# Optimization experiments

Measured on AMD Instinct MI355X. Metric: run time of the kernel, lower is better.

The kernel has to match this reference:

```python
import jax, jax.numpy as jnp
import numpy as np

B, H, W, DIM, R = 8, 64, 64, 768, 16
_DN = ('NHWC', 'HWIO', 'NHWC')


def _conv(x, k):
    # stride-1 SAME conv == torch Conv2d(padding=k//2) for 3x3 and 1x1 kernels
    return jax.lax.conv_general_dilated(x, k, (1, 1), 'SAME', dimension_numbers=_DN)


def setup_inputs() -> dict:
    key = jax.random.key(0)
    ks = jax.random.split(key, 16)
    s = 0.02
    return {
        'x': jax.random.normal(ks[0], (B, H, W, DIM), jnp.float32),
        'W_qkv': jax.random.normal(ks[1], (DIM, 3 * DIM), jnp.float32) * s,
        'b_qkv': jax.random.normal(ks[2], (3 * DIM,), jnp.float32) * s,
        'Wa_q': jax.random.normal(ks[3], (DIM, R), jnp.float32) * s,
        'Wb_q': jax.random.normal(ks[4], (R, DIM), jnp.float32) * s,
        'Wa_v': jax.random.normal(ks[5], (DIM, R), jnp.float32) * s,
        'Wb_v': jax.random.normal(ks[6], (R, DIM), jnp.float32) * s,
        'K_q3': jax.random.normal(ks[7], (3, 3, R, R), jnp.float32) * s,
        'b_q3': jax.random.normal(ks[8], (R,), jnp.float32) * s,
        'K_v3': jax.random.normal(ks[9], (3, 3, R, R), jnp.float32) * s,
        'b_v3': jax.random.normal(ks[10], (R,), jnp.float32) * s,
        'K_q1': jax.random.normal(ks[11], (1, 1, R, R), jnp.float32) * s,
        'b_q1': jax.random.normal(ks[12], (R,), jnp.float32) * s,
        'K_v1': jax.random.normal(ks[13], (1, 1, R, R), jnp.float32) * s,
        'b_v1': jax.random.normal(ks[14], (R,), jnp.float32) * s,
    }


def reference(x, W_qkv, b_qkv, Wa_q, Wb_q, Wa_v, Wb_v,
              K_q3, b_q3, K_v3, b_v3, K_q1, b_q1, K_v1, b_v1):
    dim = x.shape[-1]
    # base QKV projection: [B,H,W,3*dim]
    qkv = jnp.einsum('bhwc,cd->bhwd', x, W_qkv) + b_qkv
    # low-rank down-projections: [B,H,W,r]
    a_q = x @ Wa_q
    a_v = x @ Wa_v
    # NHWC convs replace the permute->conv->permute dance in the torch code
    mid_q = _conv(a_q, K_q3) + b_q3 + _conv(a_q, K_q1) + b_q1 + a_q
    mid_v = _conv(a_v, K_v3) + b_v3 + _conv(a_v, K_v1) + b_v1 + a_v
    new_q = mid_q @ Wb_q  # [B,H,W,dim]
    new_v = mid_v @ Wb_v
    qkv = qkv.at[..., :dim].add(new_q)
    qkv = qkv.at[..., -dim:].add(new_v)
    return qkv
```

## Files before the change

### kernel.cpp

```cpp
#include <hip/hip_runtime.h>

typedef __bf16 bf16;
typedef __attribute__((ext_vector_type(8))) __bf16 bf16x8;
typedef __attribute__((ext_vector_type(4))) float f32x4;

#define AS1U(p) ((const __attribute__((address_space(1))) unsigned int*)(p))
#define AS3U(p) ((__attribute__((address_space(3))) unsigned int*)(p))

__device__ __forceinline__ unsigned short f2bf(float f) {
    union { float f; unsigned int u; } a; a.f = f;
    unsigned int u = a.u;
    u += 0x7fffu + ((u >> 16) & 1u);
    return (unsigned short)(u >> 16);
}
__device__ __forceinline__ unsigned int pk2(float a, float b) {
    return (unsigned int)f2bf(a) | ((unsigned int)f2bf(b) << 16);
}

#define MTOT 32768
#define DIM  768
#define KP   832
#define NOUT 2304

__global__ __launch_bounds__(256) void bbuild_kernel(
    const float* __restrict__ Wqkv, const float* __restrict__ Wbq,
    const float* __restrict__ Wbv, const float* __restrict__ Waq,
    const float* __restrict__ Wav, unsigned short* __restrict__ Bt,
    unsigned short* __restrict__ WaT)
{
    const int bx = blockIdx.x;
    const int t = threadIdx.x;
    if (bx < 432) {
        __shared__ float Ts[64][65];
        const int kt = bx % 12, nt = bx / 12;
        #pragma unroll
        for (int it = 0; it < 4; ++it) {
            int idx = it * 256 + t;
            int kr = idx >> 4;
            int nc = (idx & 15) * 4;
            float4 v = *(const float4*)(Wqkv + (size_t)(kt * 64 + kr) * NOUT + nt * 64 + nc);
            Ts[kr][nc + 0] = v.x; Ts[kr][nc + 1] = v.y;
            Ts[kr][nc + 2] = v.z; Ts[kr][nc + 3] = v.w;
        }
        __syncthreads();
        #pragma unroll
        for (int it = 0; it < 4; ++it) {
            int idx = it * 256 + t;
            int nr = idx >> 4;
            int kc = (idx & 15) * 4;
            ushort4 u;
            u.x = f2bf(Ts[kc + 0][nr]); u.y = f2bf(Ts[kc + 1][nr]);
            u.z = f2bf(Ts[kc + 2][nr]); u.w = f2bf(Ts[kc + 3][nr]);
            *(ushort4*)(Bt + (size_t)(nt * 64 + nr) * KP + kt * 64 + kc) = u;
        }
    } else if (bx < 576) {
        int idx = (bx - 432) * 256 + t;
        int n = idx >> 4;
        int k = 768 + (idx & 15) * 4;
        ushort4 u;
        unsigned short* up = (unsigned short*)&u;
        #pragma unroll
        for (int j = 0; j < 4; ++j) {
            int kk = k + j;
            float v = 0.f;
            if (kk < 784) { if (n < 768) v = Wbq[(size_t)(kk - 768) * 768 + n]; }
            else if (kk < 800) { if (n >= 1536) v = Wbv[(size_t)(kk - 784) * 768 + (n - 1536)]; }
            up[j] = f2bf(v);
        }
        *(ushort4*)(Bt + (size_t)n * KP + k) = u;
    } else {
        int idx = (bx - 576) * 256 + t;
        int n = idx / 768, k = idx % 768;
        float v = (n < 16) ? Waq[(size_t)k * 16 + n] : Wav[(size_t)k * 16 + (n - 16)];
        WaT[(size_t)n * 768 + k] = f2bf(v);
    }
}

__global__ __launch_bounds__(256) void prep_kernel(
    const float* __restrict__ x, const bf16* __restrict__ WaT,
    unsigned short* __restrict__ Ap, float* __restrict__ aq, float* __restrict__ av)
{
    __shared__ bf16 Xs[64 * 64];
    const int t = threadIdx.x;
    const int wave = t >> 6, lane = t & 63;
    const int l15 = lane & 15, q = lane >> 4;
    const int p0 = blockIdx.x * 64;
    const int row = t >> 2, c16 = (t & 3) * 16;
    const int r8 = row & 7, ch0 = c16 >> 3;
    f32x4 acc[2] = {};

    for (int kt = 0; kt < 12; ++kt) {
        const float* xp = x + (size_t)(p0 + row) * DIM + kt * 64 + c16;
        float4 v0 = *(const float4*)(xp + 0);
        float4 v1 = *(const float4*)(xp + 4);
        float4 v2 = *(const float4*)(xp + 8);
        float4 v3 = *(const float4*)(xp + 12);
        uint4 u0, u1;
        u0.x = pk2(v0.x, v0.y); u0.y = pk2(v0.z, v0.w);
        u0.z = pk2(v1.x, v1.y); u0.w = pk2(v1.z, v1.w);
        u1.x = pk2(v2.x, v2.y); u1.y = pk2(v2.z, v2.w);
        u1.z = pk2(v3.x, v3.y); u1.w = pk2(v3.z, v3.w);
        unsigned short* apq = Ap + (size_t)(p0 + row) * KP + kt * 64 + c16;
        *(uint4*)(apq) = u0;
        *(uint4*)(apq + 8) = u1;
        __syncthreads();
        *(uint4*)(Xs + row * 64 + ((ch0 + 0) ^ r8) * 8) = u0;
        *(uint4*)(Xs + row * 64 + ((ch0 + 1) ^ r8) * 8) = u1;
        __syncthreads();
        bf16x8 bfr[2][2];
        #pragma unroll
        for (int kk = 0; kk < 2; ++kk)
            #pragma unroll
            for (int nf = 0; nf < 2; ++nf)
                bfr[kk][nf] = *(const bf16x8*)(WaT + (size_t)(nf * 16 + l15) * 768
                                               + kt * 64 + kk * 32 + q * 8);
        #pragma unroll
        for (int kk = 0; kk < 2; ++kk) {
            int phys = ((kk << 2) + q) ^ (l15 & 7);
            bf16x8 af = *(const bf16x8*)(Xs + (wave * 16 + l15) * 64 + phys * 8);
            acc[0] = __builtin_amdgcn_mfma_f32_16x16x32_bf16(af, bfr[kk][0], acc[0], 0, 0, 0);
            acc[1] = __builtin_amdgcn_mfma_f32_16x16x32_bf16(af, bfr[kk][1], acc[1], 0, 0, 0);
        }
    }
    const int m = wave * 16 + q * 4;
    #pragma unroll
    for (int r = 0; r < 4; ++r) {
        aq[(size_t)(p0 + m + r) * 16 + l15] = acc[0][r];
        av[(size_t)(p0 + m + r) * 16 + l15] = acc[1][r];
    }
    uint4 z; z.x = z.y = z.z = z.w = 0u;
    *(uint4*)(Ap + (size_t)(p0 + row) * KP + 800 + (t & 3) * 8) = z;
}

__global__ __launch_bounds__(256) void conv_mid_kernel(
    const float* __restrict__ aq, const float* __restrict__ av,
    const float* __restrict__ Kq3, const float* __restrict__ bq3,
    const float* __restrict__ Kv3, const float* __restrict__ bv3,
    const float* __restrict__ Kq1, const float* __restrict__ bq1,
    const float* __restrict__ Kv1, const float* __restrict__ bv1,
    unsigned short* __restrict__ Ap)
{
    const int bx = blockIdx.x;
    const int qv   = bx & 1;
    const int tile = (bx >> 1) & 15;
    const int b    = bx >> 5;
    const float* a  = qv ? av  : aq;
    const float* K3 = qv ? Kv3 : Kq3;
    const float* K1 = qv ? Kv1 : Kq1;
    const float* b3 = qv ? bv3 : bq3;
    const float* b1 = qv ? bv1 : bq1;

    __shared__ float K3s[9][16][16];
    __shared__ float K1s[16][16];
    const int t = threadIdx.x;
    for (int i = t; i < 9 * 256; i += 256) ((float*)K3s)[i] = K3[i];
    ((float*)K1s)[t] = K1[t];
    __syncthreads();

    const int lh = t >> 4, lw = t & 15;
    const int h = (tile >> 2) * 16 + lh;
    const int w = (tile & 3) * 16 + lw;

    float acc[16];
    const float* ac = a + (((size_t)b * 64 + h) * 64 + w) * 16;
    float cen[16];
    #pragma unroll
    for (int i4 = 0; i4 < 4; ++i4) {
        float4 qd = ((const float4*)ac)[i4];
        cen[i4 * 4 + 0] = qd.x; cen[i4 * 4 + 1] = qd.y;
        cen[i4 * 4 + 2] = qd.z; cen[i4 * 4 + 3] = qd.w;
    }
    #pragma unroll
    for (int o = 0; o < 16; ++o) acc[o] = b3[o] + b1[o] + cen[o];
    #pragma unroll
    for (int i = 0; i < 16; ++i) {
        float vi = cen[i];
        #pragma unroll
        for (int o = 0; o < 16; ++o) acc[o] += vi * K1s[i][o];
    }
    for (int dh = -1; dh <= 1; ++dh) {
        for (int dw = -1; dw <= 1; ++dw) {
            int hh = h + dh, ww = w + dw;
            if ((unsigned)hh < 64u && (unsigned)ww < 64u) {
                const float* ap = a + (((size_t)b * 64 + hh) * 64 + ww) * 16;
                float v[16];
                #pragma unroll
                for (int i4 = 0; i4 < 4; ++i4) {
                    float4 qd = ((const float4*)ap)[i4];
                    v[i4 * 4 + 0] = qd.x; v[i4 * 4 + 1] = qd.y;
                    v[i4 * 4 + 2] = qd.z; v[i4 * 4 + 3] = qd.w;
                }
                const int tap = (dh + 1) * 3 + (dw + 1);
                #pragma unroll
                for (int i = 0; i < 16; ++i) {
                    float vi = v[i];
                    #pragma unroll
                    for (int o = 0; o < 16; ++o) acc[o] += vi * K3s[tap][i][o];
                }
            }
        }
    }
    unsigned short* dst = Ap + (((size_t)b * 64 + h) * 64 + w) * KP + 768 + qv * 16;
    #pragma unroll
    for (int o4 = 0; o4 < 4; ++o4) {
        ushort4 u;
        u.x = f2bf(acc[o4 * 4 + 0]); u.y = f2bf(acc[o4 * 4 + 1]);
        u.z = f2bf(acc[o4 * 4 + 2]); u.w = f2bf(acc[o4 * 4 + 3]);
        *(ushort4*)(dst + o4 * 4) = u;
    }
}

__global__ __launch_bounds__(512, 2) void gemm_kernel(
    const bf16* __restrict__ A, const bf16* __restrict__ Bt,
    const float* __restrict__ bias, float* __restrict__ out)
{
    __shared__ bf16 As[2][256 * 64];
    __shared__ bf16 Bs[2][256 * 64];
    const int t = threadIdx.x;
    const int wave = t >> 6, lane = t & 63;
    const int wm = wave >> 2, wn = wave & 3;
    const int m0 = blockIdx.y * 256, n0 = blockIdx.x * 256;

    const int sr8 = lane >> 3;
    const int slc = (lane & 7) ^ sr8;
    const bf16* gA = A  + (size_t)(m0 + wave * 8 + sr8) * KP + slc * 8;
    const bf16* gB = Bt + (size_t)(n0 + wave * 8 + sr8) * KP + slc * 8;
    const int ldsbase = wave * 512 + lane * 8;

    const int l15 = lane & 15;
    const int q   = lane >> 4;
    const int l7  = lane & 7;

    f32x4 acc[8][4] = {};

    auto STAGE = [&](int kt1, int bufi) {
        const int k0 = kt1 * 64;
        #pragma unroll
        for (int it = 0; it < 4; ++it) {
            __builtin_amdgcn_global_load_lds(AS1U(gA + (size_t)(it * 64) * KP + k0),
                AS3U(&As[bufi][it * 4096 + ldsbase]), 16, 0, 0);
            __builtin_amdgcn_global_load_lds(AS1U(gB + (size_t)(it * 64) * KP + k0),
                AS3U(&Bs[bufi][it * 4096 + ldsbase]), 16, 0, 0);
        }
    };

    STAGE(0, 0);

    for (int kt = 0; kt < 13; ++kt) {
        const int cur = kt & 1;
        __builtin_amdgcn_sched_barrier(0);
        if (kt < 12) {
            STAGE(kt + 1, cur ^ 1);
            asm volatile("s_waitcnt vmcnt(8)" ::: "memory");
        } else {
            asm volatile("s_waitcnt vmcnt(0)" ::: "memory");
        }
        __builtin_amdgcn_s_barrier();

        const bf16* as = &As[cur][0];
        const bf16* bs = &Bs[cur][0];

        bf16x8 bfr[2][4];
        #pragma unroll
        for (int kk = 0; kk < 2; ++kk) {
            const int phys = ((kk << 2) + q) ^ l7;
            #pragma unroll
            for (int ni = 0; ni < 4; ++ni)
                bfr[kk][ni] = *(const bf16x8*)(bs + (wn * 64 + ni * 16 + l15) * 64 + phys * 8);
        }

        #pragma unroll
        for (int p = 0; p < 4; ++p) {
            bf16x8 af[2][2];
            #pragma unroll
            for (int j = 0; j < 2; ++j) {
                const int mi = p * 2 + j;
                #pragma unroll
                for (int kk = 0; kk < 2; ++kk) {
                    const int phys = ((kk << 2) + q) ^ l7;
                    af[j][kk] = *(const bf16x8*)(as + (wm * 128 + mi * 16 + l15) * 64 + phys * 8);
                }
            }
            __builtin_amdgcn_s_barrier();
            asm volatile("s_waitcnt lgkmcnt(0)" ::: "memory");
            __builtin_amdgcn_s_setprio(1);
            #pragma unroll
            for (int j = 0; j < 2; ++j)
                #pragma unroll
                for (int ni = 0; ni < 4; ++ni)
                    #pragma unroll
                    for (int kk = 0; kk < 2; ++kk)
                        acc[p * 2 + j][ni] = __builtin_amdgcn_mfma_f32_16x16x32_bf16(
                            af[j][kk], bfr[kk][ni], acc[p * 2 + j][ni], 0, 0, 0);
            __builtin_amdgcn_s_setprio(0);
            __builtin_amdgcn_s_barrier();
        }
    }

    #pragma unroll
    for (int ni = 0; ni < 4; ++ni) {
        const int col = n0 + wn * 64 + ni * 16 + l15;
        const float bv = bias[col];
        #pragma unroll
        for (int mi = 0; mi < 8; ++mi) {
            const int rbase = m0 + wm * 128 + mi * 16 + (q << 2);
            #pragma unroll
            for (int r = 0; r < 4; ++r)
                out[(size_t)(rbase + r) * NOUT + col] = acc[mi][ni][r] + bv;
        }
    }
}

extern "C" void kernel_launch(void* const* d_in, const int* in_sizes, int n_in,
                              void* d_out, int out_size, void* d_ws, size_t ws_size,
                              hipStream_t stream) {
    const float* x    = (const float*)d_in[0];
    const float* Wqkv = (const float*)d_in[1];
    const float* bqkv = (const float*)d_in[2];
    const float* Waq  = (const float*)d_in[3];
    const float* Wbq  = (const float*)d_in[4];
    const float* Wav  = (const float*)d_in[5];
    const float* Wbv  = (const float*)d_in[6];
    const float* Kq3  = (const float*)d_in[7];
    const float* bq3  = (const float*)d_in[8];
    const float* Kv3  = (const float*)d_in[9];
    const float* bv3  = (const float*)d_in[10];
    const float* Kq1  = (const float*)d_in[11];
    const float* bq1  = (const float*)d_in[12];
    const float* Kv1  = (const float*)d_in[13];
    const float* bv1  = (const float*)d_in[14];
    float* out = (float*)d_out;

    char* ws = (char*)d_ws;
    unsigned short* Ap  = (unsigned short*)ws;
    float* aq           = (float*)(ws + 54525952);
    float* av           = (float*)(ws + 54525952 + 2097152);
    unsigned short* Bt  = (unsigned short*)(ws + 54525952 + 4194304);
    unsigned short* WaT = (unsigned short*)(ws + 62554112);

    bbuild_kernel<<<672, 256, 0, stream>>>(Wqkv, Wbq, Wbv, Waq, Wav, Bt, WaT);
    prep_kernel<<<MTOT / 64, 256, 0, stream>>>(x, (const bf16*)WaT, Ap, aq, av);
    conv_mid_kernel<<<256, 256, 0, stream>>>(aq, av, Kq3, bq3, Kv3, bv3,
                                             Kq1, bq1, Kv1, bv1, Ap);
    gemm_kernel<<<dim3(NOUT / 256, MTOT / 256), 512, 0, stream>>>(
        (const bf16*)Ap, (const bf16*)Bt, bqkv, out);
}
```

Baseline: 601.9 us.

## Remap GEMM blocks per XCD, drop prep LDS staging and a barrier

The prep kernel no longer stages the bf16 tile of x through shared memory. Each lane now reloads its MFMA A-fragment straight from global x and converts it in registers, which removes two __syncthreads per k-step at the cost of reading x twice. The GEMM launch becomes a 1D grid of 1152 blocks, remapped so that consecutive tiles land on the same XCD and reuse its L2. One s_barrier before the MFMA cluster is replaced by a sched_barrier, which cuts synchronisation inside the k-loop.

```diff
diff --git a/kernel.cpp b/kernel.cpp
--- a/kernel.cpp
+++ b/kernel.cpp
@@ -80,13 +80,11 @@
     const float* __restrict__ x, const bf16* __restrict__ WaT,
     unsigned short* __restrict__ Ap, float* __restrict__ aq, float* __restrict__ av)
 {
-    __shared__ bf16 Xs[64 * 64];
     const int t = threadIdx.x;
     const int wave = t >> 6, lane = t & 63;
     const int l15 = lane & 15, q = lane >> 4;
     const int p0 = blockIdx.x * 64;
     const int row = t >> 2, c16 = (t & 3) * 16;
-    const int r8 = row & 7, ch0 = c16 >> 3;
     f32x4 acc[2] = {};
 
     for (int kt = 0; kt < 12; ++kt) {
@@ -103,10 +101,6 @@
         unsigned short* apq = Ap + (size_t)(p0 + row) * KP + kt * 64 + c16;
         *(uint4*)(apq) = u0;
         *(uint4*)(apq + 8) = u1;
-        __syncthreads();
-        *(uint4*)(Xs + row * 64 + ((ch0 + 0) ^ r8) * 8) = u0;
-        *(uint4*)(Xs + row * 64 + ((ch0 + 1) ^ r8) * 8) = u1;
-        __syncthreads();
         bf16x8 bfr[2][2];
         #pragma unroll
         for (int kk = 0; kk < 2; ++kk)
@@ -116,10 +110,15 @@
                                                + kt * 64 + kk * 32 + q * 8);
         #pragma unroll
         for (int kk = 0; kk < 2; ++kk) {
-            int phys = ((kk << 2) + q) ^ (l15 & 7);
-            bf16x8 af = *(const bf16x8*)(Xs + (wave * 16 + l15) * 64 + phys * 8);
-            acc[0] = __builtin_amdgcn_mfma_f32_16x16x32_bf16(af, bfr[kk][0], acc[0], 0, 0, 0);
-            acc[1] = __builtin_amdgcn_mfma_f32_16x16x32_bf16(af, bfr[kk][1], acc[1], 0, 0, 0);
+            const float* fp = x + (size_t)(p0 + wave * 16 + l15) * DIM
+                              + kt * 64 + kk * 32 + q * 8;
+            float4 a0 = *(const float4*)(fp + 0);
+            float4 a1 = *(const float4*)(fp + 4);
+            union { uint4 u; bf16x8 v; } ua;
+            ua.u.x = pk2(a0.x, a0.y); ua.u.y = pk2(a0.z, a0.w);
+            ua.u.z = pk2(a1.x, a1.y); ua.u.w = pk2(a1.z, a1.w);
+            acc[0] = __builtin_amdgcn_mfma_f32_16x16x32_bf16(ua.v, bfr[kk][0], acc[0], 0, 0, 0);
+            acc[1] = __builtin_amdgcn_mfma_f32_16x16x32_bf16(ua.v, bfr[kk][1], acc[1], 0, 0, 0);
         }
     }
     const int m = wave * 16 + q * 4;
@@ -219,7 +218,11 @@
     const int t = threadIdx.x;
     const int wave = t >> 6, lane = t & 63;
     const int wm = wave >> 2, wn = wave & 3;
-    const int m0 = blockIdx.y * 256, n0 = blockIdx.x * 256;
+
+    const int lb = blockIdx.x;
+    const int xcd = lb & 7, c = lb >> 3;
+    const int g = xcd * 144 + c;
+    const int m0 = (g / 9) * 256, n0 = (g % 9) * 256;
 
     const int sr8 = lane >> 3;
     const int slc = (lane & 7) ^ sr8;
@@ -227,9 +230,7 @@
     const bf16* gB = Bt + (size_t)(n0 + wave * 8 + sr8) * KP + slc * 8;
     const int ldsbase = wave * 512 + lane * 8;
 
-    const int l15 = lane & 15;
-    const int q   = lane >> 4;
-    const int l7  = lane & 7;
+    const int l15 = lane & 15, q = lane >> 4, l7 = lane & 7;
 
     f32x4 acc[8][4] = {};
 
@@ -281,8 +282,8 @@
                     af[j][kk] = *(const bf16x8*)(as + (wm * 128 + mi * 16 + l15) * 64 + phys * 8);
                 }
             }
-            __builtin_amdgcn_s_barrier();
             asm volatile("s_waitcnt lgkmcnt(0)" ::: "memory");
+            __builtin_amdgcn_sched_barrier(0);
             __builtin_amdgcn_s_setprio(1);
             #pragma unroll
             for (int j = 0; j < 2; ++j)
@@ -342,6 +343,6 @@
     prep_kernel<<<MTOT / 64, 256, 0, stream>>>(x, (const bf16*)WaT, Ap, aq, av);
     conv_mid_kernel<<<256, 256, 0, stream>>>(aq, av, Kq3, bq3, Kv3, bv3,
                                              Kq1, bq1, Kv1, bv1, Ap);
-    gemm_kernel<<<dim3(NOUT / 256, MTOT / 256), 512, 0, stream>>>(
+    gemm_kernel<<<1152, 512, 0, stream>>>(
         (const bf16*)Ap, (const bf16*)Bt, bqkv, out);
 }
```

Result: no change. 598.3 us (-0.6%).
